# Optimization experiments

Hardware: AMD Instinct MI355X
Metric: run time of the kernel (lower is better)

The kernel has to match this reference:

```python
import jax, jax.numpy as jnp
import numpy as np

KERNEL_SIZE = 9
STRIDE = 1
LN_EPS = 1e-5


def _toeplitz(L, dtype):
    # T[t, l] = 1 iff l - t == STRIDE * i for i in range(KERNEL_SIZE // STRIDE)
    d = jnp.arange(L)[None, :] - jnp.arange(L)[:, None]
    mask = (d >= 0) & (d % STRIDE == 0) & ((d // STRIDE) < (KERNEL_SIZE // STRIDE))
    return mask.astype(dtype)


def setup_inputs() -> dict:
    key = jax.random.key(0)
    ks = jax.random.split(key, 4)
    N, Cin, L, V = 16, 256, 300, 25
    P, Cout = 3, 256
    x = jax.random.normal(ks[0], (N, Cin, L, V), dtype=jnp.float32)
    A = jax.random.uniform(ks[1], (P, V, V), dtype=jnp.float32)
    conv_w = jax.random.normal(ks[2], (Cout * P, Cin), dtype=jnp.float32) * 0.02
    conv_b = jax.random.normal(ks[3], (Cout * P,), dtype=jnp.float32) * 0.02
    ln_gamma = jnp.ones((Cout, 1, V), dtype=jnp.float32)
    ln_beta = jnp.zeros((Cout, 1, V), dtype=jnp.float32)
    edge_importance = jnp.ones((P, V * V), dtype=jnp.float32)
    return {"x": x, "A": A, "conv_w": conv_w, "conv_b": conv_b,
            "ln_gamma": ln_gamma, "ln_beta": ln_beta,
            "edge_importance": edge_importance}


def reference(x, A, conv_w, conv_b, ln_gamma, ln_beta, edge_importance):
    N, Cin, L, V = x.shape
    P = A.shape[0]
    Cout = conv_w.shape[0] // P

    res = x  # in_channels == out_channels and stride == 1 -> identity residual

    # 1x1 conv -> (N, Cout*P, L, V); split into P chunks of Cout along channels
    y = jnp.einsum('nclv,oc->nolv', x, conv_w) + conv_b[None, :, None, None]
    y = y.reshape(N, P, Cout, L, V)  # chunk p == channels [p*Cout:(p+1)*Cout]

    # partitioned graph aggregation with edge importance: (P,V,V) adjacency
    Aw = A * edge_importance.reshape(P, V, V)
    y = jnp.einsum('npclv,pvw->npclw', y, Aw)  # (N, P, Cout, L, V)

    # temporal conv via toeplitz matmul over frame dim L
    T = _toeplitz(L, y.dtype)
    y = jnp.einsum('npclv,lm->npcmv', y, T)  # (N, P, Cout, L, V)

    # sum over partitions -> (N, Cout, L, V)
    y = y.sum(axis=1)

    # LayerNorm over (C, V) per (n, l), affine params shaped (Cout, 1, V)
    mu = jnp.mean(y, axis=(1, 3), keepdims=True)
    var = jnp.var(y, axis=(1, 3), keepdims=True)
    y = (y - mu) * jax.lax.rsqrt(var + LN_EPS)
    y = y * ln_gamma[None] + ln_beta[None]
    y = jax.nn.relu(y)

    # residual add, final ReLU (dropout rate 0.0 -> identity)
    return jax.nn.relu(y + res)
```

## Files before the change

### kernel.cpp

```cpp
#include <hip/hip_runtime.h>

#define NN 16
#define CIN 256
#define COUT 256
#define LL 300
#define VV 25
#define VP 28
#define PP 3
#define KS 9
#define KK 768
#define MM (NN*LL*VV)
#define MPAD 120064
#define MBLK 938
#define XCDS 8
#define MPX 38

typedef float floatx4 __attribute__((ext_vector_type(4)));
typedef short short8 __attribute__((ext_vector_type(8)));

__device__ __forceinline__ unsigned short f2bf(float f) {
    unsigned u = __builtin_bit_cast(unsigned, f);
    u += 0x7fff + ((u >> 16) & 1);
    return (unsigned short)(u >> 16);
}
__device__ __forceinline__ float bf2f(unsigned short h) {
    unsigned u = ((unsigned)h) << 16;
    return __builtin_bit_cast(float, u);
}
__device__ __forceinline__ void gl2lds16(const void* g, void* l) {
    __builtin_amdgcn_global_load_lds(
        (const __attribute__((address_space(1))) void*)g,
        (__attribute__((address_space(3))) void*)l, 16, 0, 0);
}

__global__ __launch_bounds__(256) void k_prep(
    const float* __restrict__ A, const float* __restrict__ conv_w,
    const float* __restrict__ conv_b, const float* __restrict__ ei,
    unsigned short* __restrict__ w2t, float* __restrict__ bias2,
    unsigned short* __restrict__ xa)
{
    const int t = blockIdx.x * 256 + threadIdx.x;
    const int nthr = gridDim.x * 256;
    for (int idx = t; idx < COUT * KK; idx += nthr) {
        int c = idx / KK, k = idx % KK, p = k >> 8, ci = k & 255;
        w2t[idx] = f2bf(conv_w[(p * COUT + c) * CIN + ci]);
    }
    for (int idx = t; idx < COUT * VV; idx += nthr) {
        int c = idx / VV, w = idx % VV;
        float s = 0.f;
        for (int p = 0; p < PP; ++p) {
            float cs = 0.f;
            for (int v = 0; v < VV; ++v) {
                int a = (p * VV + v) * VV + w;
                cs += A[a] * ei[a];
            }
            s += conv_b[p * COUT + c] * cs;
        }
        bias2[idx] = s;
    }
    for (int idx = t; idx < (MPAD - MM) * KK; idx += nthr)
        xa[(size_t)MM * KK + idx] = 0;
}

__global__ __launch_bounds__(256) void k_agg(
    const float* __restrict__ x, const float* __restrict__ A,
    const float* __restrict__ ei, unsigned short* __restrict__ xa)
{
    __shared__ float AwL[PP * VV * VP];
    const int l = blockIdx.x, n = blockIdx.y, t = threadIdx.x;
    for (int idx = t; idx < PP * VV * VV; idx += 256) {
        int pv = idx / VV, w = idx % VV;
        AwL[pv * VP + w] = A[idx] * ei[idx];
    }
    __syncthreads();

    float xv[VV];
    const float* xp = x + ((size_t)(n * CIN + t) * LL + l) * VV;
    #pragma unroll
    for (int v = 0; v < VV; ++v) xv[v] = xp[v];

    const size_t mrow = (size_t)(n * LL + l) * VV;
    #pragma unroll
    for (int p = 0; p < PP; ++p) {
        float acc[VV];
        #pragma unroll
        for (int w = 0; w < VV; ++w) acc[w] = 0.f;
        #pragma unroll
        for (int v = 0; v < VV; ++v) {
            const float xvv = xv[v];
            const float* ar = &AwL[(p * VV + v) * VP];
            #pragma unroll
            for (int wq = 0; wq < 24; wq += 4) {
                const float4 f = *(const float4*)(ar + wq);
                acc[wq + 0] += xvv * f.x; acc[wq + 1] += xvv * f.y;
                acc[wq + 2] += xvv * f.z; acc[wq + 3] += xvv * f.w;
            }
            acc[24] += xvv * ar[24];
        }
        #pragma unroll
        for (int w = 0; w < VV; ++w)
            xa[(mrow + w) * KK + p * CIN + t] = f2bf(acc[w]);
    }
}

__global__ __launch_bounds__(256) void k_gemm(
    const unsigned short* __restrict__ xa,
    const unsigned short* __restrict__ w2t,
    unsigned short* __restrict__ z)
{
    __shared__ __align__(16) unsigned short As[128 * 32];
    __shared__ __align__(16) unsigned short Bs[128 * 32];
    const int t = threadIdx.x, wv = t >> 6, ln = t & 63;
    const int m0 = blockIdx.x * 128, c0 = blockIdx.y * 128;

    floatx4 acc[4][4];
    #pragma unroll
    for (int i = 0; i < 4; ++i)
        #pragma unroll
        for (int j = 0; j < 4; ++j)
            acc[i][j] = (floatx4){0.f, 0.f, 0.f, 0.f};

    const int srow = wv * 32 + (ln >> 2);
    const int scol = (ln & 3) * 8;
    const int mw = (wv >> 1) * 64, nw = (wv & 1) * 64;
    const int frow = ln & 15, fcol = (ln >> 4) * 8;

    for (int kt = 0; kt < KK / 32; ++kt) {
        const int k0 = kt * 32;
        __syncthreads();
        gl2lds16(xa  + (size_t)(m0 + srow)      * KK + k0 + scol, &As[(wv * 32) * 32]);
        gl2lds16(xa  + (size_t)(m0 + srow + 16) * KK + k0 + scol, &As[(wv * 32 + 16) * 32]);
        gl2lds16(w2t + (size_t)(c0 + srow)      * KK + k0 + scol, &Bs[(wv * 32) * 32]);
        gl2lds16(w2t + (size_t)(c0 + srow + 16) * KK + k0 + scol, &Bs[(wv * 32 + 16) * 32]);
        __syncthreads();

        short8 af[4], bf[4];
        #pragma unroll
        for (int i = 0; i < 4; ++i)
            af[i] = *(const short8*)&As[(mw + i * 16 + frow) * 32 + fcol];
        #pragma unroll
        for (int j = 0; j < 4; ++j)
            bf[j] = *(const short8*)&Bs[(nw + j * 16 + frow) * 32 + fcol];
        #pragma unroll
        for (int i = 0; i < 4; ++i)
            #pragma unroll
            for (int j = 0; j < 4; ++j)
                acc[i][j] = __builtin_amdgcn_mfma_f32_16x16x32_bf16(af[i], bf[j], acc[i][j], 0, 0, 0);
    }

    const int q = ln >> 4, cL = ln & 15;
    #pragma unroll
    for (int i = 0; i < 4; ++i) {
        #pragma unroll
        for (int j = 0; j < 4; ++j) {
            #pragma unroll
            for (int r = 0; r < 4; ++r) {
                const int m = m0 + mw + i * 16 + q * 4 + r;
                const int c = c0 + nw + j * 16 + cL;
                if (m < MM) z[(size_t)m * COUT + c] = f2bf(acc[i][j][r]);
            }
        }
    }
}

__global__ __launch_bounds__(256) void k_ln(
    const unsigned short* __restrict__ z, const float* __restrict__ x,
    const float* __restrict__ bias2, const float* __restrict__ gamma,
    const float* __restrict__ beta, float* __restrict__ out)
{
    const int b = blockIdx.x;
    const int g = b & (XCDS - 1);
    const int r = b >> 3;
    const int mi = r % MPX;
    const int n = r / MPX;
    const int m = g * MPX + mi;
    if (m >= LL) return;
    const int t = threadIdx.x;

    float zw[VV];
    #pragma unroll
    for (int w = 0; w < VV; ++w) zw[w] = 0.f;

    const int l0 = (m >= KS - 1) ? (m - (KS - 1)) : 0;
    for (int l = l0; l <= m; ++l) {
        const unsigned short* zp = z + (size_t)((n * LL + l) * VV) * COUT + t;
        #pragma unroll
        for (int w = 0; w < VV; ++w) zw[w] += bf2f(zp[(size_t)w * COUT]);
    }
    const float cnt = (float)(m - l0 + 1);
    const float* b2 = bias2 + t * VV;
    #pragma unroll
    for (int w = 0; w < VV; ++w) zw[w] += cnt * b2[w];

    float s1 = 0.f, s2 = 0.f;
    #pragma unroll
    for (int w = 0; w < VV; ++w) { s1 += zw[w]; s2 += zw[w] * zw[w]; }

    __shared__ float rs[4], rq[4], stats[2];
    #pragma unroll
    for (int off = 32; off; off >>= 1) { s1 += __shfl_down(s1, off); s2 += __shfl_down(s2, off); }
    const int wid = t >> 6, lane = t & 63;
    if (lane == 0) { rs[wid] = s1; rq[wid] = s2; }
    __syncthreads();
    if (t == 0) {
        const float S1 = rs[0] + rs[1] + rs[2] + rs[3];
        const float S2 = rq[0] + rq[1] + rq[2] + rq[3];
        const float inv = 1.f / (COUT * VV);
        const float mu = S1 * inv;
        const float var = S2 * inv - mu * mu;
        stats[0] = mu;
        stats[1] = rsqrtf(var + 1e-5f);
    }
    __syncthreads();
    const float mu = stats[0], rsd = stats[1];

    const float* gp = gamma + t * VV;
    const float* bp = beta + t * VV;
    const float* xp = x + ((size_t)(n * CIN + t) * LL + m) * VV;
    float* op = out + ((size_t)(n * COUT + t) * LL + m) * VV;
    #pragma unroll
    for (int w = 0; w < VV; ++w) {
        float val = (zw[w] - mu) * rsd * gp[w] + bp[w];
        val = fmaxf(val, 0.f);
        val += xp[w];
        op[w] = fmaxf(val, 0.f);
    }
}

extern "C" void kernel_launch(void* const* d_in, const int* in_sizes, int n_in,
                              void* d_out, int out_size, void* d_ws, size_t ws_size,
                              hipStream_t stream) {
    const float* x      = (const float*)d_in[0];
    const float* A      = (const float*)d_in[1];
    const float* conv_w = (const float*)d_in[2];
    const float* conv_b = (const float*)d_in[3];
    const float* gamma  = (const float*)d_in[4];
    const float* beta   = (const float*)d_in[5];
    const float* ei     = (const float*)d_in[6];
    float* out = (float*)d_out;

    char* ws = (char*)d_ws;
    unsigned short* xa  = (unsigned short*)ws;
    unsigned short* z   = (unsigned short*)(ws + 184418304);
    unsigned short* w2t = (unsigned short*)(ws + 245891072);
    float*          b2  = (float*)(ws + 246284288);

    k_prep<<<64, 256, 0, stream>>>(A, conv_w, conv_b, ei, w2t, b2, xa);
    k_agg<<<dim3(LL, NN), 256, 0, stream>>>(x, A, ei, xa);
    k_gemm<<<dim3(MBLK, 2), 256, 0, stream>>>(xa, w2t, z);
    k_ln<<<XCDS * NN * MPX, 256, 0, stream>>>(z, x, b2, gamma, beta, out);
}
```

Measured before the change: 557.6 us.

## Process two frames per LayerNorm block and remap GEMM blocks per XCD

```diff
diff --git a/kernel.cpp b/kernel.cpp
--- a/kernel.cpp
+++ b/kernel.cpp
@@ -13,7 +13,10 @@
 #define MPAD 120064
 #define MBLK 938
 #define XCDS 8
-#define MPX 38
+#define NLP 150
+#define LPX 19
+#define GWID (2*MBLK)
+#define GPX 235
 
 typedef float floatx4 __attribute__((ext_vector_type(4)));
 typedef short short8 __attribute__((ext_vector_type(8)));
@@ -36,7 +39,7 @@
 __global__ __launch_bounds__(256) void k_prep(
     const float* __restrict__ A, const float* __restrict__ conv_w,
     const float* __restrict__ conv_b, const float* __restrict__ ei,
-    unsigned short* __restrict__ w2t, float* __restrict__ bias2,
+    unsigned short* __restrict__ w2t, float* __restrict__ b2t,
     unsigned short* __restrict__ xa)
 {
     const int t = blockIdx.x * 256 + threadIdx.x;
@@ -56,7 +59,7 @@
             }
             s += conv_b[p * COUT + c] * cs;
         }
-        bias2[idx] = s;
+        b2t[w * COUT + c] = s;
     }
     for (int idx = t; idx < (MPAD - MM) * KK; idx += nthr)
         xa[(size_t)MM * KK + idx] = 0;
@@ -110,8 +113,12 @@
 {
     __shared__ __align__(16) unsigned short As[128 * 32];
     __shared__ __align__(16) unsigned short Bs[128 * 32];
+    const int bid = blockIdx.x;
+    const int g = bid & (XCDS - 1), sidx = bid >> 3;
+    const int wid = g * GPX + sidx;
+    if (wid >= GWID) return;
+    const int m0 = (wid >> 1) * 128, c0 = (wid & 1) * 128;
     const int t = threadIdx.x, wv = t >> 6, ln = t & 63;
-    const int m0 = blockIdx.x * 128, c0 = blockIdx.y * 128;
 
     floatx4 acc[4][4];
     #pragma unroll
@@ -165,65 +172,111 @@
 
 __global__ __launch_bounds__(256) void k_ln(
     const unsigned short* __restrict__ z, const float* __restrict__ x,
-    const float* __restrict__ bias2, const float* __restrict__ gamma,
+    const float* __restrict__ b2t, const float* __restrict__ gamma,
     const float* __restrict__ beta, float* __restrict__ out)
 {
+    __shared__ __align__(16) float ylds[2][VV * COUT];
+    __shared__ float red[4][4];
+    __shared__ float stats[4];
+
     const int b = blockIdx.x;
     const int g = b & (XCDS - 1);
     const int r = b >> 3;
-    const int mi = r % MPX;
-    const int n = r / MPX;
-    const int m = g * MPX + mi;
-    if (m >= LL) return;
+    const int li = r % LPX;
+    const int n  = r / LPX;
+    const int lp = g * LPX + li;
+    if (lp >= NLP) return;
+    const int l0 = lp * 2;
     const int t = threadIdx.x;
 
-    float zw[VV];
-    #pragma unroll
-    for (int w = 0; w < VV; ++w) zw[w] = 0.f;
-
-    const int l0 = (m >= KS - 1) ? (m - (KS - 1)) : 0;
-    for (int l = l0; l <= m; ++l) {
-        const unsigned short* zp = z + (size_t)((n * LL + l) * VV) * COUT + t;
-        #pragma unroll
-        for (int w = 0; w < VV; ++w) zw[w] += bf2f(zp[(size_t)w * COUT]);
-    }
-    const float cnt = (float)(m - l0 + 1);
-    const float* b2 = bias2 + t * VV;
-    #pragma unroll
-    for (int w = 0; w < VV; ++w) zw[w] += cnt * b2[w];
-
-    float s1 = 0.f, s2 = 0.f;
-    #pragma unroll
-    for (int w = 0; w < VV; ++w) { s1 += zw[w]; s2 += zw[w] * zw[w]; }
-
-    __shared__ float rs[4], rq[4], stats[2];
-    #pragma unroll
-    for (int off = 32; off; off >>= 1) { s1 += __shfl_down(s1, off); s2 += __shfl_down(s2, off); }
+    float s10 = 0.f, s20 = 0.f, s11 = 0.f, s21 = 0.f;
+    const size_t zrow0 = (size_t)(n * LL) * (VV * COUT);
+
+    #pragma unroll
+    for (int i = 0; i < 4; ++i) {
+        const int vs = t + 256 * i;
+        if (i < 3 || t < 32) {
+            float f[10][8];
+            #pragma unroll
+            for (int j = 0; j < 10; ++j) {
+                const int lr = l0 - 8 + j;
+                if (lr >= 0) {
+                    const short8 rv = *(const short8*)(z + zrow0 + (size_t)lr * (VV * COUT) + vs * 8);
+                    #pragma unroll
+                    for (int k = 0; k < 8; ++k) f[j][k] = bf2f((unsigned short)rv[k]);
+                } else {
+                    #pragma unroll
+                    for (int k = 0; k < 8; ++k) f[j][k] = 0.f;
+                }
+            }
+            const float cnt0 = (float)(((l0     < 8) ? l0     : 8) + 1);
+            const float cnt1 = (float)(((l0 + 1 < 8) ? l0 + 1 : 8) + 1);
+            const float4 ba = *(const float4*)(b2t + vs * 8);
+            const float4 bb = *(const float4*)(b2t + vs * 8 + 4);
+            const float bv[8] = {ba.x, ba.y, ba.z, ba.w, bb.x, bb.y, bb.z, bb.w};
+            float y0[8], y1[8];
+            #pragma unroll
+            for (int k = 0; k < 8; ++k) {
+                float smid = f[1][k];
+                #pragma unroll
+                for (int j = 2; j < 9; ++j) smid += f[j][k];
+                const float a = smid + f[0][k] + cnt0 * bv[k];
+                const float c = smid + f[9][k] + cnt1 * bv[k];
+                y0[k] = a; y1[k] = c;
+                s10 += a; s20 += a * a;
+                s11 += c; s21 += c * c;
+            }
+            *(float4*)&ylds[0][vs * 8]     = (float4){y0[0], y0[1], y0[2], y0[3]};
+            *(float4*)&ylds[0][vs * 8 + 4] = (float4){y0[4], y0[5], y0[6], y0[7]};
+            *(float4*)&ylds[1][vs * 8]     = (float4){y1[0], y1[1], y1[2], y1[3]};
+            *(float4*)&ylds[1][vs * 8 + 4] = (float4){y1[4], y1[5], y1[6], y1[7]};
+        }
+    }
+
+    #pragma unroll
+    for (int off = 32; off; off >>= 1) {
+        s10 += __shfl_down(s10, off);
+        s20 += __shfl_down(s20, off);
+        s11 += __shfl_down(s11, off);
+        s21 += __shfl_down(s21, off);
+    }
     const int wid = t >> 6, lane = t & 63;
-    if (lane == 0) { rs[wid] = s1; rq[wid] = s2; }
+    if (lane == 0) { red[wid][0] = s10; red[wid][1] = s20; red[wid][2] = s11; red[wid][3] = s21; }
     __syncthreads();
     if (t == 0) {
-        const float S1 = rs[0] + rs[1] + rs[2] + rs[3];
-        const float S2 = rq[0] + rq[1] + rq[2] + rq[3];
+        float S1 = 0.f, S2 = 0.f, T1 = 0.f, T2 = 0.f;
+        #pragma unroll
+        for (int w2 = 0; w2 < 4; ++w2) { S1 += red[w2][0]; S2 += red[w2][1]; T1 += red[w2][2]; T2 += red[w2][3]; }
         const float inv = 1.f / (COUT * VV);
-        const float mu = S1 * inv;
-        const float var = S2 * inv - mu * mu;
-        stats[0] = mu;
-        stats[1] = rsqrtf(var + 1e-5f);
+        float mu = S1 * inv, var = S2 * inv - mu * mu;
+        stats[0] = mu; stats[1] = rsqrtf(var + 1e-5f);
+        mu = T1 * inv; var = T2 * inv - mu * mu;
+        stats[2] = mu; stats[3] = rsqrtf(var + 1e-5f);
     }
     __syncthreads();
-    const float mu = stats[0], rsd = stats[1];
-
-    const float* gp = gamma + t * VV;
-    const float* bp = beta + t * VV;
-    const float* xp = x + ((size_t)(n * CIN + t) * LL + m) * VV;
-    float* op = out + ((size_t)(n * COUT + t) * LL + m) * VV;
+
+    const float mu0 = stats[0], rsd0 = stats[1], mu1 = stats[2], rsd1 = stats[3];
+    const int c = t;
+    const float* gp = gamma + c * VV;
+    const float* bp = beta  + c * VV;
+    const float* xp = x   + ((size_t)(n * CIN  + c) * (LL * VV)) + l0 * VV;
+    float*       op = out + ((size_t)(n * COUT + c) * (LL * VV)) + l0 * VV;
+    float val[2 * VV];
     #pragma unroll
     for (int w = 0; w < VV; ++w) {
-        float val = (zw[w] - mu) * rsd * gp[w] + bp[w];
-        val = fmaxf(val, 0.f);
-        val += xp[w];
-        op[w] = fmaxf(val, 0.f);
+        const float gw = gp[w], bw = bp[w];
+        const float v0 = (ylds[0][w * COUT + c] - mu0) * rsd0 * gw + bw;
+        const float v1 = (ylds[1][w * COUT + c] - mu1) * rsd1 * gw + bw;
+        val[w]      = fmaxf(v0, 0.f);
+        val[VV + w] = fmaxf(v1, 0.f);
+    }
+    #pragma unroll
+    for (int k = 0; k < VV; ++k) {
+        const float2 xv = *(const float2*)(xp + 2 * k);
+        float2 o;
+        o.x = fmaxf(val[2 * k]     + xv.x, 0.f);
+        o.y = fmaxf(val[2 * k + 1] + xv.y, 0.f);
+        *(float2*)(op + 2 * k) = o;
     }
 }
 
@@ -247,6 +300,6 @@
 
     k_prep<<<64, 256, 0, stream>>>(A, conv_w, conv_b, ei, w2t, b2, xa);
     k_agg<<<dim3(LL, NN), 256, 0, stream>>>(x, A, ei, xa);
-    k_gemm<<<dim3(MBLK, 2), 256, 0, stream>>>(xa, w2t, z);
-    k_ln<<<XCDS * NN * MPX, 256, 0, stream>>>(z, x, b2, gamma, beta, out);
-}
+    k_gemm<<<XCDS * GPX, 256, 0, stream>>>(xa, w2t, z);
+    k_ln<<<XCDS * LPX * NN, 256, 0, stream>>>(z, x, b2, gamma, beta, out);
+}
```

Measured after the change: 547.9 us. About the same (-1.7%).
